# Kernel optimization log

Measured on AMD Instinct MI355X. Metric: run time of the kernel, lower is better.

The kernel has to match this reference:

```python
import jax, jax.numpy as jnp
import numpy as np

B, S = 2, 1024
V, D, H, L, F, M = 50257, 768, 12, 6, 3072, 1024
DK = D // H
EPS = 1e-5


def _layer_norm(x, g, b):
    mu = jnp.mean(x, axis=-1, keepdims=True)
    var = jnp.mean(jnp.square(x - mu), axis=-1, keepdims=True)
    return (x - mu) * jax.lax.rsqrt(var + EPS) * g + b


def setup_inputs() -> dict:
    key = jax.random.key(0)
    ks = jax.random.split(key, 20)
    std = 0.02
    inp = {
        'input_ids': jax.random.randint(ks[0], (B, S), 0, V),
        'tok_emb': jax.random.normal(ks[1], (V, D), jnp.float32) * std,
        'pos_emb': jax.random.normal(ks[2], (M, D), jnp.float32) * std,
        # per-layer stacked params; linear weights stored as [in, out] (y = x @ W)
        'wq': jax.random.normal(ks[3], (L, D, D), jnp.float32) * std,
        'wk': jax.random.normal(ks[4], (L, D, D), jnp.float32) * std,
        'wv': jax.random.normal(ks[5], (L, D, D), jnp.float32) * std,
        'wo': jax.random.normal(ks[6], (L, D, D), jnp.float32) * std,
        'bo': jnp.zeros((L, D), jnp.float32),
        'fc_w': jax.random.normal(ks[7], (L, D, F), jnp.float32) * std,
        'fc_b': jnp.zeros((L, F), jnp.float32),
        'proj_w': jax.random.normal(ks[8], (L, F, D), jnp.float32) * std,
        'proj_b': jnp.zeros((L, D), jnp.float32),
        'ln1_g': jnp.ones((L, D), jnp.float32),
        'ln1_b': jnp.zeros((L, D), jnp.float32),
        'ln2_g': jnp.ones((L, D), jnp.float32),
        'ln2_b': jnp.zeros((L, D), jnp.float32),
        'lnf_g': jnp.ones((D,), jnp.float32),
        'lnf_b': jnp.zeros((D,), jnp.float32),
        'out_w': jax.random.normal(ks[9], (D, V), jnp.float32) * std,
    }
    return inp


def reference(input_ids, tok_emb, pos_emb, wq, wk, wv, wo, bo, fc_w, fc_b,
              proj_w, proj_b, ln1_g, ln1_b, ln2_g, ln2_b, lnf_g, lnf_b, out_w):
    b, s = input_ids.shape
    x = tok_emb[input_ids] + pos_emb[jnp.arange(s)][None, :, :]  # [B,S,D]
    causal = jnp.tril(jnp.ones((s, s), bool))  # [S,S]
    scale = 1.0 / np.sqrt(DK)
    for l in range(L):
        xn = _layer_norm(x, ln1_g[l], ln1_b[l])
        q = (xn @ wq[l]).reshape(b, s, H, DK).transpose(0, 2, 1, 3)
        k = (xn @ wk[l]).reshape(b, s, H, DK).transpose(0, 2, 1, 3)
        v = (xn @ wv[l]).reshape(b, s, H, DK).transpose(0, 2, 1, 3)
        scores = jnp.einsum('bhqd,bhkd->bhqk', q, k) * scale
        scores = jnp.where(causal[None, None], scores, -1e9)
        attn = jax.nn.softmax(scores, axis=-1)
        ctx = jnp.einsum('bhqk,bhkd->bhqd', attn, v)
        ctx = ctx.transpose(0, 2, 1, 3).reshape(b, s, D)
        x = x + ctx @ wo[l] + bo[l]
        xn = _layer_norm(x, ln2_g[l], ln2_b[l])
        h = jax.nn.gelu(xn @ fc_w[l] + fc_b[l], approximate=False)
        x = x + h @ proj_w[l] + proj_b[l]
    x = _layer_norm(x, lnf_g, lnf_b)
    logits = x @ out_w  # [B,S,V]
    return logits
```

## Files before the change

### kernel.cpp

```cpp
#include <hip/hip_runtime.h>
#include <hip/hip_bf16.h>
#include <math.h>

#define BB 2
#define SS 1024
#define DD 768
#define HH 12
#define LL 6
#define FF 3072
#define VV 50257
#define DKK 64
#define NROWS (BB * SS)
#define QKVN (3 * DD)
#define QBLK 64
#define KVBLK 64
#define VPAD 50432

#define OFF_QKV 0
#define OFF_WO  1769472
#define OFF_FC  2359296
#define OFF_PROJ 4718592
#define PL      7077888

typedef __attribute__((ext_vector_type(8))) short short8v;
typedef __attribute__((ext_vector_type(4))) float f32x4;
typedef __attribute__((ext_vector_type(4))) int int4v;

__device__ __forceinline__ float gelu_f(float x) {
    return 0.5f * x * (1.0f + erff(x * 0.70710678118654752440f));
}

__device__ __forceinline__ void gload16(const void* g, void* l) {
    __builtin_amdgcn_global_load_lds(
        (const __attribute__((address_space(1))) void*)g,
        (__attribute__((address_space(3))) void*)l, 16, 0, 0);
}
__device__ __forceinline__ unsigned lds_off(const void* p) {
    return (unsigned)(size_t)(const __attribute__((address_space(3))) char*)p;
}
__device__ __forceinline__ short8v ds_read128(unsigned addr) {
    short8v r;
    asm volatile("ds_read_b128 %0, %1" : "=v"(r) : "v"(addr));
    return r;
}

__global__ __launch_bounds__(256) void embed_kernel(
    const int* __restrict__ ids, const float* __restrict__ tok,
    const float* __restrict__ pos, float* __restrict__ x) {
    int row = blockIdx.x;
    int s = row & (SS - 1);
    int id = ids[row];
    const float* t = tok + (size_t)id * DD;
    const float* p = pos + (size_t)s * DD;
    float* xr = x + (size_t)row * DD;
    for (int i = threadIdx.x; i < DD; i += 256)
        xr[i] = t[i] + p[i];
}

__global__ __launch_bounds__(256) void ln_kernel(
    const float* __restrict__ x, const float* __restrict__ g,
    const float* __restrict__ b, float* __restrict__ out) {
    int row = blockIdx.x;
    int tid = threadIdx.x;
    const float* xr = x + (size_t)row * DD;
    float v0 = xr[tid], v1 = xr[tid + 256], v2 = xr[tid + 512];
    __shared__ float red[256];
    red[tid] = v0 + v1 + v2;
    __syncthreads();
    for (int s2 = 128; s2 > 0; s2 >>= 1) {
        if (tid < s2) red[tid] += red[tid + s2];
        __syncthreads();
    }
    float mu = red[0] * (1.0f / DD);
    __syncthreads();
    float d0 = v0 - mu, d1 = v1 - mu, d2 = v2 - mu;
    red[tid] = d0 * d0 + d1 * d1 + d2 * d2;
    __syncthreads();
    for (int s2 = 128; s2 > 0; s2 >>= 1) {
        if (tid < s2) red[tid] += red[tid + s2];
        __syncthreads();
    }
    float r = rsqrtf(red[0] * (1.0f / DD) + 1e-5f);
    float* o = out + (size_t)row * DD;
    o[tid]       = d0 * r * g[tid]       + b[tid];
    o[tid + 256] = d1 * r * g[tid + 256] + b[tid + 256];
    o[tid + 512] = d2 * r * g[tid + 512] + b[tid + 512];
}

__global__ __launch_bounds__(256) void ln_bf16_kernel(
    const float* __restrict__ x, const float* __restrict__ g,
    const float* __restrict__ b, __hip_bfloat16* __restrict__ out) {
    int row = blockIdx.x;
    int tid = threadIdx.x;
    const float* xr = x + (size_t)row * DD;
    float v0 = xr[tid], v1 = xr[tid + 256], v2 = xr[tid + 512];
    __shared__ float red[256];
    red[tid] = v0 + v1 + v2;
    __syncthreads();
    for (int s2 = 128; s2 > 0; s2 >>= 1) {
        if (tid < s2) red[tid] += red[tid + s2];
        __syncthreads();
    }
    float mu = red[0] * (1.0f / DD);
    __syncthreads();
    float d0 = v0 - mu, d1 = v1 - mu, d2 = v2 - mu;
    red[tid] = d0 * d0 + d1 * d1 + d2 * d2;
    __syncthreads();
    for (int s2 = 128; s2 > 0; s2 >>= 1) {
        if (tid < s2) red[tid] += red[tid + s2];
        __syncthreads();
    }
    float r = rsqrtf(red[0] * (1.0f / DD) + 1e-5f);
    __hip_bfloat16* o = out + (size_t)row * DD;
    o[tid]       = __float2bfloat16(d0 * r * g[tid]       + b[tid]);
    o[tid + 256] = __float2bfloat16(d1 * r * g[tid + 256] + b[tid + 256]);
    o[tid + 512] = __float2bfloat16(d2 * r * g[tid + 512] + b[tid + 512]);
}

__global__ __launch_bounds__(256) void transpose_cvt_kernel(
    const float* __restrict__ W, __hip_bfloat16* __restrict__ Wt, int K, int N) {
    __shared__ float t[32][33];
    int bn = blockIdx.x * 32, bk = blockIdx.y * 32;
    int tx = threadIdx.x & 31, ty = threadIdx.x >> 5;
    for (int r = ty; r < 32; r += 8)
        t[r][tx] = (bn + tx < N) ? W[(size_t)(bk + r) * N + bn + tx] : 0.0f;
    __syncthreads();
    for (int r = ty; r < 32; r += 8) {
        int n = bn + r;
        if (n < N) Wt[(size_t)n * K + bk + tx] = __float2bfloat16(t[tx][r]);
    }
}

__global__ __launch_bounds__(256) void transpose_all_kernel(
    const float* __restrict__ wq, const float* __restrict__ wk,
    const float* __restrict__ wv, const float* __restrict__ wo,
    const float* __restrict__ fc_w, const float* __restrict__ proj_w,
    const float* __restrict__ out_w, __hip_bfloat16* __restrict__ Wt_all) {
    int bid = blockIdx.x;
    const float* W;
    __hip_bfloat16* Wt;
    int K, N, tn, tk;
    if (bid < 6 * 6912) {
        int l = bid / 6912, r = bid % 6912;
        __hip_bfloat16* base = Wt_all + (size_t)l * PL;
        if (r < 1728) {
            int which = r / 576, idx = r % 576;
            W = (which == 0 ? wq : (which == 1 ? wk : wv)) + (size_t)l * DD * DD;
            Wt = base + (size_t)which * DD * DD;
            K = DD; N = DD; tn = idx % 24; tk = idx / 24;
        } else if (r < 2304) {
            int idx = r - 1728;
            W = wo + (size_t)l * DD * DD;
            Wt = base + OFF_WO;
            K = DD; N = DD; tn = idx % 24; tk = idx / 24;
        } else if (r < 4608) {
            int idx = r - 2304;
            W = fc_w + (size_t)l * DD * FF;
            Wt = base + OFF_FC;
            K = DD; N = FF; tn = idx % 96; tk = idx / 96;
        } else {
            int idx = r - 4608;
            W = proj_w + (size_t)l * FF * DD;
            Wt = base + OFF_PROJ;
            K = FF; N = DD; tn = idx % 24; tk = idx / 24;
        }
    } else {
        int idx = bid - 6 * 6912;
        W = out_w;
        Wt = Wt_all + (size_t)6 * PL;
        K = DD; N = VV; tn = idx % 1571; tk = idx / 1571;
    }
    __shared__ float t[32][33];
    int bn = tn * 32, bk = tk * 32;
    int tx = threadIdx.x & 31, ty = threadIdx.x >> 5;
    for (int r = ty; r < 32; r += 8)
        t[r][tx] = (bn + tx < N) ? W[(size_t)(bk + r) * N + bn + tx] : 0.0f;
    __syncthreads();
    for (int r = ty; r < 32; r += 8) {
        int n = bn + r;
        if (n < N) Wt[(size_t)n * K + bk + tx] = __float2bfloat16(t[tx][r]);
    }
}

#define LDSOFF(row, ks) (((row) * 64) + ((((ks) ^ (((row) >> 1) & 3))) << 4))
#define SWZ128(row, byteoff) \
    ((row) * 128 + (((((byteoff) >> 4) ^ ((row) & 7)) & 7) << 4) + ((byteoff) & 15))

__device__ __forceinline__ void tile_remap(int mtiles, int BM, int BN, int& bm, int& bn) {
    const int nblk = gridDim.x;
    int hw = blockIdx.x, j = hw;
    if ((nblk & 7) == 0) j = (hw & 7) * (nblk >> 3) + (hw >> 3);
    bm = (j % mtiles) * BM;
    bn = (j / mtiles) * BN;
}

__global__ __launch_bounds__(512) void gemm256_kernel(
    const __hip_bfloat16* __restrict__ A, const __hip_bfloat16* __restrict__ Wt,
    const float* __restrict__ bias, float* __restrict__ Cf,
    __hip_bfloat16* __restrict__ Cb, int M, int N, int K, int do_gelu, int mtiles) {
    __shared__ __align__(16) char lds[131072];
    const int tid = threadIdx.x;
    const int lane = tid & 63;
    const int w = tid >> 6;
    const int wr = w >> 2, wc = w & 3;
    const int r16 = lane & 15, kg = lane >> 4;
    int bm, bn;
    tile_remap(mtiles, 256, 256, bm, bn);

    auto STAGE = [&](int T) {
        char* lb = lds + (T & 3) * 32768;
        int k0 = T * 32;
#pragma unroll
        for (int u = 0; u < 2; ++u) {
            int cb = w * 128 + u * 64;
            int c = cb + lane;
            int row = c >> 2;
            int sc = ((c & 3) ^ ((row >> 1) & 3)) * 8;
            gload16(A + (size_t)(bm + row) * K + k0 + sc, lb + cb * 16);
            gload16(Wt + (size_t)(bn + row) * K + k0 + sc, lb + 16384 + cb * 16);
        }
    };

    f32x4 acc[8][4];
    const f32x4 zf = {0.0f, 0.0f, 0.0f, 0.0f};
#pragma unroll
    for (int i = 0; i < 8; ++i)
#pragma unroll
        for (int j = 0; j < 4; ++j) acc[i][j] = zf;

    unsigned aoff[8], boff[4];
#pragma unroll
    for (int i = 0; i < 8; ++i) aoff[i] = LDSOFF(wr * 128 + i * 16 + r16, kg);
#pragma unroll
    for (int j = 0; j < 4; ++j) boff[j] = 16384 + LDSOFF(wc * 64 + j * 16 + r16, kg);
    const unsigned lbase = lds_off(lds);

    STAGE(0); STAGE(1); STAGE(2);
    const int NT = K >> 5;
    for (int t = 0; t < NT; ++t) {
        if (t < NT - 2)       asm volatile("s_waitcnt vmcnt(8)" ::: "memory");
        else if (t == NT - 2) asm volatile("s_waitcnt vmcnt(4)" ::: "memory");
        else                  asm volatile("s_waitcnt vmcnt(0)" ::: "memory");
        __builtin_amdgcn_s_barrier();
        __builtin_amdgcn_sched_barrier(0);
        if (t + 3 < NT) STAGE(t + 3);
        unsigned ab = lbase + (unsigned)(t & 3) * 32768u;
        short8v bf[4], af[8];
#pragma unroll
        for (int j = 0; j < 4; ++j) bf[j] = ds_read128(ab + boff[j]);
#pragma unroll
        for (int i = 0; i < 8; ++i) af[i] = ds_read128(ab + aoff[i]);
#pragma unroll
        for (int i = 0; i < 8; ++i) {
            asm volatile("s_waitcnt lgkmcnt(%0)" :: "i"(7 - i) : "memory");
            __builtin_amdgcn_sched_barrier(0);
#pragma unroll
            for (int j = 0; j < 4; ++j)
                acc[i][j] = __builtin_amdgcn_mfma_f32_16x16x32_bf16(
                    af[i], bf[j], acc[i][j], 0, 0, 0);
        }
    }

    const int rg = lane >> 4;
#pragma unroll
    for (int i = 0; i < 8; ++i)
#pragma unroll
        for (int j = 0; j < 4; ++j) {
            int col = bn + wc * 64 + j * 16 + r16;
            if (col < N) {
#pragma unroll
                for (int r = 0; r < 4; ++r) {
                    int row = bm + wr * 128 + i * 16 + rg * 4 + r;
                    float v = acc[i][j][r];
                    if (bias) v += bias[col];
                    if (do_gelu) v = gelu_f(v);
                    if (Cf) Cf[(size_t)row * N + col] = v;
                    else Cb[(size_t)row * N + col] = __float2bfloat16(v);
                }
            }
        }
}

template<int BM, int BN>
__global__ __launch_bounds__(256) void gemm_mfma_kernel(
    const __hip_bfloat16* __restrict__ A, const __hip_bfloat16* __restrict__ Wt,
    const float* __restrict__ bias, const float* __restrict__ residual,
    float* __restrict__ Cf, __hip_bfloat16* __restrict__ Cb,
    int M, int N, int K, int do_gelu, int mtiles) {
    constexpr int BK = 32;
    constexpr int UA = (BM * 4) / 256;
    constexpr int UB = (BN * 4) / 256;
    constexpr int FM = BM / 32;
    constexpr int FN = BN / 32;
    __shared__ __align__(16) char As[BM * 64];
    __shared__ __align__(16) char Bs[BN * 64];

    const int tid = threadIdx.x;
    const int lane = tid & 63;
    const int wid = tid >> 6;
    int bm, bn;
    tile_remap(mtiles, BM, BN, bm, bn);
    const int r16 = lane & 15;
    const int kg = lane >> 4;
    const int wm = (wid >> 1) * (FM * 16);
    const int wn = (wid & 1) * (FN * 16);

    f32x4 acc[FM][FN];
    const f32x4 zf = {0.0f, 0.0f, 0.0f, 0.0f};
#pragma unroll
    for (int i = 0; i < FM; ++i)
#pragma unroll
        for (int j = 0; j < FN; ++j) acc[i][j] = zf;

    int4v areg[UA], breg[UB];
    const int4v zi = {0, 0, 0, 0};

#pragma unroll
    for (int u = 0; u < UA; ++u) {
        int c = tid + u * 256, row = c >> 2, sl = c & 3;
        areg[u] = *(const int4v*)(A + (size_t)(bm + row) * K + sl * 8);
    }
#pragma unroll
    for (int u = 0; u < UB; ++u) {
        int c = tid + u * 256, row = c >> 2, sl = c & 3;
        int4v bv = zi;
        if (bn + row < N) bv = *(const int4v*)(Wt + (size_t)(bn + row) * K + sl * 8);
        breg[u] = bv;
    }

    for (int k0 = 0; k0 < K; k0 += BK) {
        __syncthreads();
#pragma unroll
        for (int u = 0; u < UA; ++u) {
            int c = tid + u * 256, row = c >> 2, sl = c & 3;
            *(int4v*)(As + LDSOFF(row, sl)) = areg[u];
        }
#pragma unroll
        for (int u = 0; u < UB; ++u) {
            int c = tid + u * 256, row = c >> 2, sl = c & 3;
            *(int4v*)(Bs + LDSOFF(row, sl)) = breg[u];
        }
        __syncthreads();
        int kn = k0 + BK;
        if (kn < K) {
#pragma unroll
            for (int u = 0; u < UA; ++u) {
                int c = tid + u * 256, row = c >> 2, sl = c & 3;
                areg[u] = *(const int4v*)(A + (size_t)(bm + row) * K + kn + sl * 8);
            }
#pragma unroll
            for (int u = 0; u < UB; ++u) {
                int c = tid + u * 256, row = c >> 2, sl = c & 3;
                int4v bv = zi;
                if (bn + row < N) bv = *(const int4v*)(Wt + (size_t)(bn + row) * K + kn + sl * 8);
                breg[u] = bv;
            }
        }
        short8v af[FM], bfr[FN];
#pragma unroll
        for (int i = 0; i < FM; ++i) {
            int row = wm + i * 16 + r16;
            af[i] = *(const short8v*)(As + LDSOFF(row, kg));
        }
#pragma unroll
        for (int j = 0; j < FN; ++j) {
            int row = wn + j * 16 + r16;
            bfr[j] = *(const short8v*)(Bs + LDSOFF(row, kg));
        }
#pragma unroll
        for (int i = 0; i < FM; ++i)
#pragma unroll
            for (int j = 0; j < FN; ++j)
                acc[i][j] = __builtin_amdgcn_mfma_f32_16x16x32_bf16(
                    af[i], bfr[j], acc[i][j], 0, 0, 0);
    }

    const int rg = lane >> 4;
#pragma unroll
    for (int i = 0; i < FM; ++i) {
#pragma unroll
        for (int j = 0; j < FN; ++j) {
            int col = bn + wn + j * 16 + r16;
            if (col < N) {
#pragma unroll
                for (int r = 0; r < 4; ++r) {
                    int row = bm + wm + i * 16 + rg * 4 + r;
                    float v = acc[i][j][r];
                    if (bias) v += bias[col];
                    if (do_gelu) v = gelu_f(v);
                    size_t o = (size_t)row * N + col;
                    if (residual) v += residual[o];
                    if (Cf) Cf[o] = v;
                    else Cb[o] = __float2bfloat16(v);
                }
            }
        }
    }
}

__global__ __launch_bounds__(256) void qkv_gemm_kernel(
    const __hip_bfloat16* __restrict__ A, const __hip_bfloat16* __restrict__ Wt,
    __hip_bfloat16* __restrict__ qh, __hip_bfloat16* __restrict__ kh,
    __hip_bfloat16* __restrict__ vt) {
    constexpr int BM = 128, BN = 128, BK = 32;
    constexpr int K = DD;
    constexpr int FM = 4, FN = 4;
    __shared__ __align__(16) char As[BM * 64];
    __shared__ __align__(16) char Bs[BN * 64];

    const int tid = threadIdx.x;
    const int lane = tid & 63;
    const int wid = tid >> 6;
    int bm, bn;
    tile_remap(16, BM, BN, bm, bn);
    const int r16 = lane & 15;
    const int kg = lane >> 4;
    const int wm = (wid >> 1) * 64;
    const int wn = (wid & 1) * 64;

    f32x4 acc[FM][FN];
    const f32x4 zf = {0.0f, 0.0f, 0.0f, 0.0f};
#pragma unroll
    for (int i = 0; i < FM; ++i)
#pragma unroll
        for (int j = 0; j < FN; ++j) acc[i][j] = zf;

    int4v areg[2], breg[2];
#pragma unroll
    for (int u = 0; u < 2; ++u) {
        int c = tid + u * 256, row = c >> 2, sl = c & 3;
        areg[u] = *(const int4v*)(A + (size_t)(bm + row) * K + sl * 8);
        breg[u] = *(const int4v*)(Wt + (size_t)(bn + row) * K + sl * 8);
    }

    for (int k0 = 0; k0 < K; k0 += BK) {
        __syncthreads();
#pragma unroll
        for (int u = 0; u < 2; ++u) {
            int c = tid + u * 256, row = c >> 2, sl = c & 3;
            *(int4v*)(As + LDSOFF(row, sl)) = areg[u];
            *(int4v*)(Bs + LDSOFF(row, sl)) = breg[u];
        }
        __syncthreads();
        int kn = k0 + BK;
        if (kn < K) {
#pragma unroll
            for (int u = 0; u < 2; ++u) {
                int c = tid + u * 256, row = c >> 2, sl = c & 3;
                areg[u] = *(const int4v*)(A + (size_t)(bm + row) * K + kn + sl * 8);
                breg[u] = *(const int4v*)(Wt + (size_t)(bn + row) * K + kn + sl * 8);
            }
        }
        short8v af[FM], bfr[FN];
#pragma unroll
        for (int i = 0; i < FM; ++i)
            af[i] = *(const short8v*)(As + LDSOFF(wm + i * 16 + r16, kg));
#pragma unroll
        for (int j = 0; j < FN; ++j)
            bfr[j] = *(const short8v*)(Bs + LDSOFF(wn + j * 16 + r16, kg));
#pragma unroll
        for (int i = 0; i < FM; ++i)
#pragma unroll
            for (int j = 0; j < FN; ++j)
                acc[i][j] = __builtin_amdgcn_mfma_f32_16x16x32_bf16(
                    af[i], bfr[j], acc[i][j], 0, 0, 0);
    }

#pragma unroll
    for (int i = 0; i < FM; ++i) {
#pragma unroll
        for (int j = 0; j < FN; ++j) {
            int col = bn + wn + j * 16 + r16;
#pragma unroll
            for (int r = 0; r < 4; ++r) {
                int row = bm + wm + i * 16 + kg * 4 + r;
                int b = row >> 10, s = row & (SS - 1);
                float v = acc[i][j][r];
                if (col < DD) {
                    int h = col >> 6, d = col & 63;
                    qh[((size_t)(b * HH + h) * SS + s) * DKK + d] =
                        __float2bfloat16(v * 0.125f);
                } else if (col < 2 * DD) {
                    int c = col - DD, h = c >> 6, d = c & 63;
                    kh[((size_t)(b * HH + h) * SS + s) * DKK + d] = __float2bfloat16(v);
                } else {
                    int c = col - 2 * DD, h = c >> 6, d = c & 63;
                    vt[((size_t)(b * HH + h) * DKK + d) * SS + s] = __float2bfloat16(v);
                }
            }
        }
    }
}

__global__ __launch_bounds__(256) void flash_attn_kernel(
    const __hip_bfloat16* __restrict__ qh, const __hip_bfloat16* __restrict__ kh,
    const __hip_bfloat16* __restrict__ vt, __hip_bfloat16* __restrict__ ctx) {
    __shared__ __align__(16) char Ks[KVBLK * 128];
    __shared__ __align__(16) char Vs[DKK * 128];
    __shared__ __align__(16) char Ps[4][16 * 128];

    const int bh = blockIdx.x;
    const int qt = (gridDim.y - 1) - blockIdx.y;
    const int q0 = qt * QBLK;
    const int b = bh / HH;
    const int h = bh - b * HH;
    const int tid = threadIdx.x;
    const int lane = tid & 63;
    const int w = tid >> 6;
    const int r16 = lane & 15;
    const int kg = lane >> 4;
    char* Pw = Ps[w];

    const size_t qbase = ((size_t)bh * SS + q0 + w * 16 + r16) * DKK;
    short8v qf0 = *(const short8v*)(qh + qbase + kg * 8);
    short8v qf1 = *(const short8v*)(qh + qbase + 32 + kg * 8);

    f32x4 acc_o[4];
    const f32x4 zf = {0.0f, 0.0f, 0.0f, 0.0f};
    float m[4], l[4];
#pragma unroll
    for (int j = 0; j < 4; ++j) acc_o[j] = zf;
#pragma unroll
    for (int r = 0; r < 4; ++r) { m[r] = -1e30f; l[r] = 0.0f; }

    const int nt = qt + 1;
    for (int t = 0; t < nt; ++t) {
        __syncthreads();
        {
            const __hip_bfloat16* kp = kh + ((size_t)bh * SS + t * KVBLK) * DKK;
            const __hip_bfloat16* vp = vt + (size_t)bh * DKK * SS + t * KVBLK;
#pragma unroll
            for (int u = 0; u < 2; ++u) {
                int c = tid + u * 256;
                int row = c >> 3, slot = c & 7;
                *(int4v*)(Ks + SWZ128(row, slot * 16)) =
                    *(const int4v*)(kp + (size_t)row * DKK + slot * 8);
                *(int4v*)(Vs + SWZ128(row, slot * 16)) =
                    *(const int4v*)(vp + (size_t)row * SS + slot * 8);
            }
        }
        __syncthreads();

        f32x4 s[4];
#pragma unroll
        for (int j = 0; j < 4; ++j) s[j] = zf;
#pragma unroll
        for (int j = 0; j < 4; ++j) {
            short8v k0f = *(const short8v*)(Ks + SWZ128(j * 16 + r16, kg * 16));
            short8v k1f = *(const short8v*)(Ks + SWZ128(j * 16 + r16, 64 + kg * 16));
            s[j] = __builtin_amdgcn_mfma_f32_16x16x32_bf16(qf0, k0f, s[j], 0, 0, 0);
            s[j] = __builtin_amdgcn_mfma_f32_16x16x32_bf16(qf1, k1f, s[j], 0, 0, 0);
        }

        if (t == qt) {
#pragma unroll
            for (int j = 0; j < 4; ++j)
#pragma unroll
                for (int r = 0; r < 4; ++r)
                    if (j * 16 + r16 > w * 16 + kg * 4 + r) s[j][r] = -1e30f;
        }

        float alpha[4], rsum[4];
#pragma unroll
        for (int r = 0; r < 4; ++r) {
            float v = fmaxf(fmaxf(s[0][r], s[1][r]), fmaxf(s[2][r], s[3][r]));
#pragma unroll
            for (int d2 = 1; d2 < 16; d2 <<= 1)
                v = fmaxf(v, __shfl_xor(v, d2));
            float mnew = fmaxf(m[r], v);
            alpha[r] = __expf(m[r] - mnew);
            m[r] = mnew;
            rsum[r] = 0.0f;
        }
#pragma unroll
        for (int j = 0; j < 4; ++j)
#pragma unroll
            for (int r = 0; r < 4; ++r) {
                float p = __expf(s[j][r] - m[r]);
                rsum[r] += p;
                *(__hip_bfloat16*)(Pw + SWZ128(kg * 4 + r, (j * 16 + r16) * 2)) =
                    __float2bfloat16(p);
            }
#pragma unroll
        for (int r = 0; r < 4; ++r) {
#pragma unroll
            for (int d2 = 1; d2 < 16; d2 <<= 1)
                rsum[r] += __shfl_xor(rsum[r], d2);
            l[r] = l[r] * alpha[r] + rsum[r];
        }
#pragma unroll
        for (int j = 0; j < 4; ++j)
#pragma unroll
            for (int r = 0; r < 4; ++r) acc_o[j][r] *= alpha[r];

        short8v pa0 = *(const short8v*)(Pw + SWZ128(r16, kg * 16));
        short8v pa1 = *(const short8v*)(Pw + SWZ128(r16, 64 + kg * 16));
#pragma unroll
        for (int j = 0; j < 4; ++j) {
            short8v v0f = *(const short8v*)(Vs + SWZ128(j * 16 + r16, kg * 16));
            short8v v1f = *(const short8v*)(Vs + SWZ128(j * 16 + r16, 64 + kg * 16));
            acc_o[j] = __builtin_amdgcn_mfma_f32_16x16x32_bf16(pa0, v0f, acc_o[j], 0, 0, 0);
            acc_o[j] = __builtin_amdgcn_mfma_f32_16x16x32_bf16(pa1, v1f, acc_o[j], 0, 0, 0);
        }
    }

#pragma unroll
    for (int r = 0; r < 4; ++r) {
        float inv = 1.0f / l[r];
        int row = q0 + w * 16 + kg * 4 + r;
        __hip_bfloat16* cp = ctx + ((size_t)(b * SS) + row) * DD + h * DKK;
#pragma unroll
        for (int j = 0; j < 4; ++j)
            cp[j * 16 + r16] = __float2bfloat16(acc_o[j][r] * inv);
    }
}

__global__ __launch_bounds__(256) void gemm_kernel(
    const float* __restrict__ A, const float* __restrict__ W,
    const float* __restrict__ bias, const float* __restrict__ residual,
    float* __restrict__ C, int M, int N, int K, int do_gelu) {
    __shared__ float As[16][64];
    __shared__ float Ws[16][68];
    int tid = threadIdx.x;
    int bn = blockIdx.x * 64, bm = blockIdx.y * 64;
    int tx = tid & 15, ty = tid >> 4;
    int ar = tid >> 2, ak = (tid & 3) << 2;
    int wr = tid >> 4, wc = (tid & 15) << 2;
    bool n_vec = ((N & 3) == 0);
    float acc[4][4] = {};
    for (int k0 = 0; k0 < K; k0 += 16) {
        float4 av = *(const float4*)&A[(size_t)(bm + ar) * K + (k0 + ak)];
        As[ak + 0][ar] = av.x; As[ak + 1][ar] = av.y;
        As[ak + 2][ar] = av.z; As[ak + 3][ar] = av.w;
        int gn = bn + wc;
        const float* wp = &W[(size_t)(k0 + wr) * N + gn];
        float w0, w1, w2, w3;
        if (n_vec && gn + 3 < N) {
            float4 wv4 = *(const float4*)wp;
            w0 = wv4.x; w1 = wv4.y; w2 = wv4.z; w3 = wv4.w;
        } else {
            w0 = (gn + 0 < N) ? wp[0] : 0.0f;
            w1 = (gn + 1 < N) ? wp[1] : 0.0f;
            w2 = (gn + 2 < N) ? wp[2] : 0.0f;
            w3 = (gn + 3 < N) ? wp[3] : 0.0f;
        }
        Ws[wr][wc + 0] = w0; Ws[wr][wc + 1] = w1;
        Ws[wr][wc + 2] = w2; Ws[wr][wc + 3] = w3;
        __syncthreads();
#pragma unroll
        for (int kk = 0; kk < 16; ++kk) {
            float a[4], w[4];
#pragma unroll
            for (int i = 0; i < 4; ++i) a[i] = As[kk][ty * 4 + i];
#pragma unroll
            for (int j = 0; j < 4; ++j) w[j] = Ws[kk][tx * 4 + j];
#pragma unroll
            for (int i = 0; i < 4; ++i)
#pragma unroll
                for (int j = 0; j < 4; ++j)
                    acc[i][j] = fmaf(a[i], w[j], acc[i][j]);
        }
        __syncthreads();
    }
#pragma unroll
    for (int i = 0; i < 4; ++i) {
        int row = bm + ty * 4 + i;
#pragma unroll
        for (int j = 0; j < 4; ++j) {
            int col = bn + tx * 4 + j;
            if (col < N) {
                float val = acc[i][j];
                if (bias) val += bias[col];
                if (do_gelu) val = gelu_f(val);
                if (residual) val += residual[(size_t)row * N + col];
                C[(size_t)row * N + col] = val;
            }
        }
    }
}

__global__ __launch_bounds__(256) void attn_kernel(
    const float* __restrict__ q, const float* __restrict__ k,
    const float* __restrict__ v, float* __restrict__ ctx) {
    int bid = blockIdx.x;
    int qi = bid & (SS - 1);
    int bh = bid >> 10;
    int h = bh % HH;
    int b = bh / HH;
    int tid = threadIdx.x;
    __shared__ float qs[DKK];
    __shared__ float p[SS];
    __shared__ float red[256];
    __shared__ float ctx_red[4][DKK];
    const float* qrow = q + ((size_t)(b * SS + qi)) * DD + h * DKK;
    if (tid < DKK) qs[tid] = qrow[tid];
    __syncthreads();
    int nk = qi + 1;
    const float scale = 0.125f;
    for (int ki = tid; ki < nk; ki += 256) {
        const float* krow = k + ((size_t)(b * SS + ki)) * DD + h * DKK;
        float dot = 0.0f;
#pragma unroll
        for (int d = 0; d < DKK; d += 4) {
            float4 kv = *(const float4*)&krow[d];
            dot += qs[d] * kv.x + qs[d + 1] * kv.y + qs[d + 2] * kv.z + qs[d + 3] * kv.w;
        }
        p[ki] = dot * scale;
    }
    __syncthreads();
    float lmax = -1e30f;
    for (int ki = tid; ki < nk; ki += 256) lmax = fmaxf(lmax, p[ki]);
    red[tid] = lmax;
    __syncthreads();
    for (int s2 = 128; s2 > 0; s2 >>= 1) {
        if (tid < s2) red[tid] = fmaxf(red[tid], red[tid + s2]);
        __syncthreads();
    }
    float mm = red[0];
    __syncthreads();
    float lsum = 0.0f;
    for (int ki = tid; ki < nk; ki += 256) {
        float e = __expf(p[ki] - mm);
        p[ki] = e;
        lsum += e;
    }
    red[tid] = lsum;
    __syncthreads();
    for (int s2 = 128; s2 > 0; s2 >>= 1) {
        if (tid < s2) red[tid] += red[tid + s2];
        __syncthreads();
    }
    float inv = 1.0f / red[0];
    int d = tid & 63;
    int chunk = tid >> 6;
    float accd = 0.0f;
    for (int ki = chunk; ki < nk; ki += 4)
        accd += p[ki] * v[((size_t)(b * SS + ki)) * DD + h * DKK + d];
    ctx_red[chunk][d] = accd;
    __syncthreads();
    if (tid < DKK) {
        float sum = (ctx_red[0][tid] + ctx_red[1][tid]) + (ctx_red[2][tid] + ctx_red[3][tid]);
        ctx[((size_t)(b * SS + qi)) * DD + h * DKK + tid] = sum * inv;
    }
}

extern "C" void kernel_launch(void* const* d_in, const int* in_sizes, int n_in,
                              void* d_out, int out_size, void* d_ws, size_t ws_size,
                              hipStream_t stream) {
    const int*   ids    = (const int*)  d_in[0];
    const float* tok    = (const float*)d_in[1];
    const float* pos    = (const float*)d_in[2];
    const float* wq     = (const float*)d_in[3];
    const float* wk     = (const float*)d_in[4];
    const float* wv     = (const float*)d_in[5];
    const float* wo     = (const float*)d_in[6];
    const float* bo     = (const float*)d_in[7];
    const float* fc_w   = (const float*)d_in[8];
    const float* fc_b   = (const float*)d_in[9];
    const float* proj_w = (const float*)d_in[10];
    const float* proj_b = (const float*)d_in[11];
    const float* ln1_g  = (const float*)d_in[12];
    const float* ln1_b  = (const float*)d_in[13];
    const float* ln2_g  = (const float*)d_in[14];
    const float* ln2_b  = (const float*)d_in[15];
    const float* lnf_g  = (const float*)d_in[16];
    const float* lnf_b  = (const float*)d_in[17];
    const float* out_w  = (const float*)d_in[18];
    float* out = (float*)d_out;

    dim3 blk(256);

    const size_t SZ_X    = (size_t)NROWS * DD * 4;
    const size_t SZ_XN   = (size_t)NROWS * DD * 2;
    const size_t SZ_HD   = (size_t)BB * HH * SS * DKK * 2;
    const size_t SZ_CTX  = (size_t)NROWS * DD * 2;
    const size_t SZ_H    = (size_t)NROWS * FF * 2;
    const size_t SZ_WT1  = (size_t)VPAD * DD * 2;
    const size_t SZ_WTA  = ((size_t)6 * PL + (size_t)VPAD * DD) * 2;
    const size_t ACT     = SZ_X + SZ_XN + 3 * SZ_HD + SZ_CTX + SZ_H;
    const size_t NEED_MID = ACT + SZ_WT1;
    const size_t NEED_BIG = ACT + SZ_WTA;

    if (ws_size >= NEED_MID) {
        const bool big = (ws_size >= NEED_BIG);
        char* p = (char*)d_ws;
        float*          x    = (float*)p;          p += SZ_X;
        __hip_bfloat16* xn   = (__hip_bfloat16*)p; p += SZ_XN;
        __hip_bfloat16* qhb  = (__hip_bfloat16*)p; p += SZ_HD;
        __hip_bfloat16* khb  = (__hip_bfloat16*)p; p += SZ_HD;
        __hip_bfloat16* vtb  = (__hip_bfloat16*)p; p += SZ_HD;
        __hip_bfloat16* ctx  = (__hip_bfloat16*)p; p += SZ_CTX;
        __hip_bfloat16* hbuf = (__hip_bfloat16*)p; p += SZ_H;
        __hip_bfloat16* Wt   = (__hip_bfloat16*)p;

        dim3 tD(DD / 32, DD / 32);
        dim3 tF(FF / 32, DD / 32);
        dim3 tP(DD / 32, FF / 32);
        dim3 tV((VV + 31) / 32, DD / 32);

        const int nQKV = (QKVN / 128) * (NROWS / 128);
        const int nWO  = (DD / 64) * (NROWS / 64);
        const int nFC  = (FF / 128) * (NROWS / 128);
        const int nV   = (VPAD / 256) * (NROWS / 256);
        dim3 gA(BB * HH, SS / QBLK);

        if (big)
            transpose_all_kernel<<<6 * 6912 + 37704, blk, 0, stream>>>(
                wq, wk, wv, wo, fc_w, proj_w, out_w, Wt);

        embed_kernel<<<NROWS, blk, 0, stream>>>(ids, tok, pos, x);

        for (int l = 0; l < LL; ++l) {
            __hip_bfloat16* qkvWt = big ? Wt + (size_t)l * PL : Wt;
            __hip_bfloat16* woWt  = big ? Wt + (size_t)l * PL + OFF_WO : Wt;
            __hip_bfloat16* fcWt  = big ? Wt + (size_t)l * PL + OFF_FC : Wt;
            __hip_bfloat16* pjWt  = big ? Wt + (size_t)l * PL + OFF_PROJ : Wt;

            ln_bf16_kernel<<<NROWS, blk, 0, stream>>>(x, ln1_g + l * DD, ln1_b + l * DD, xn);
            if (!big) {
                transpose_cvt_kernel<<<tD, blk, 0, stream>>>(wq + (size_t)l * DD * DD, qkvWt, DD, DD);
                transpose_cvt_kernel<<<tD, blk, 0, stream>>>(wk + (size_t)l * DD * DD, qkvWt + (size_t)DD * DD, DD, DD);
                transpose_cvt_kernel<<<tD, blk, 0, stream>>>(wv + (size_t)l * DD * DD, qkvWt + (size_t)2 * DD * DD, DD, DD);
            }
            qkv_gemm_kernel<<<nQKV, blk, 0, stream>>>(xn, qkvWt, qhb, khb, vtb);
            flash_attn_kernel<<<gA, blk, 0, stream>>>(qhb, khb, vtb, ctx);
            if (!big)
                transpose_cvt_kernel<<<tD, blk, 0, stream>>>(wo + (size_t)l * DD * DD, woWt, DD, DD);
            gemm_mfma_kernel<64, 64><<<nWO, blk, 0, stream>>>(
                ctx, woWt, bo + l * DD, x, x, nullptr, NROWS, DD, DD, 0, NROWS / 64);
            ln_bf16_kernel<<<NROWS, blk, 0, stream>>>(x, ln2_g + l * DD, ln2_b + l * DD, xn);
            if (!big)
                transpose_cvt_kernel<<<tF, blk, 0, stream>>>(fc_w + (size_t)l * DD * FF, fcWt, DD, FF);
            gemm_mfma_kernel<128, 128><<<nFC, blk, 0, stream>>>(
                xn, fcWt, fc_b + l * FF, nullptr, nullptr, hbuf, NROWS, FF, DD, 1, NROWS / 128);
            if (!big)
                transpose_cvt_kernel<<<tP, blk, 0, stream>>>(proj_w + (size_t)l * FF * DD, pjWt, FF, DD);
            gemm_mfma_kernel<64, 64><<<nWO, blk, 0, stream>>>(
                hbuf, pjWt, proj_b + l * DD, x, x, nullptr, NROWS, DD, FF, 0, NROWS / 64);
        }

        __hip_bfloat16* outWt = big ? Wt + (size_t)6 * PL : Wt;
        ln_bf16_kernel<<<NROWS, blk, 0, stream>>>(x, lnf_g, lnf_b, xn);
        if (!big)
            transpose_cvt_kernel<<<tV, blk, 0, stream>>>(out_w, outWt, DD, VV);
        gemm256_kernel<<<nV, 512, 0, stream>>>(
            xn, outWt, nullptr, out, nullptr, NROWS, VV, DD, 0, NROWS / 256);
        return;
    }

    const size_t XSZ = (size_t)NROWS * DD;
    float* ws = (float*)d_ws;
    float* x  = ws;
    float* xn = x  + XSZ;
    float* qb = xn + XSZ;
    float* kb = qb + XSZ;
    float* vb = kb + XSZ;
    float* cb = vb + XSZ;
    float* hb = cb + XSZ;

    dim3 gD((DD + 63) / 64, NROWS / 64);
    dim3 gF((FF + 63) / 64, NROWS / 64);
    dim3 gV2((VV + 63) / 64, NROWS / 64);

    embed_kernel<<<NROWS, blk, 0, stream>>>(ids, tok, pos, x);
    for (int l = 0; l < LL; ++l) {
        const float* wq_l = wq + (size_t)l * DD * DD;
        const float* wk_l = wk + (size_t)l * DD * DD;
        const float* wv_l = wv + (size_t)l * DD * DD;
        const float* wo_l = wo + (size_t)l * DD * DD;
        const float* fc_w_l = fc_w + (size_t)l * DD * FF;
        const float* pj_w_l = proj_w + (size_t)l * FF * DD;
        ln_kernel<<<NROWS, blk, 0, stream>>>(x, ln1_g + l * DD, ln1_b + l * DD, xn);
        gemm_kernel<<<gD, blk, 0, stream>>>(xn, wq_l, nullptr, nullptr, qb, NROWS, DD, DD, 0);
        gemm_kernel<<<gD, blk, 0, stream>>>(xn, wk_l, nullptr, nullptr, kb, NROWS, DD, DD, 0);
        gemm_kernel<<<gD, blk, 0, stream>>>(xn, wv_l, nullptr, nullptr, vb, NROWS, DD, DD, 0);
        attn_kernel<<<BB * HH * SS, blk, 0, stream>>>(qb, kb, vb, cb);
        gemm_kernel<<<gD, blk, 0, stream>>>(cb, wo_l, bo + l * DD, x, x, NROWS, DD, DD, 0);
        ln_kernel<<<NROWS, blk, 0, stream>>>(x, ln2_g + l * DD, ln2_b + l * DD, xn);
        gemm_kernel<<<gF, blk, 0, stream>>>(xn, fc_w_l, fc_b + l * FF, nullptr, hb, NROWS, FF, DD, 1);
        gemm_kernel<<<gD, blk, 0, stream>>>(hb, pj_w_l, proj_b + l * DD, x, x, NROWS, DD, FF, 0);
    }
    ln_kernel<<<NROWS, blk, 0, stream>>>(x, lnf_g, lnf_b, xn);
    gemm_kernel<<<gV2, blk, 0, stream>>>(xn, out_w, nullptr, nullptr, out, NROWS, VV, DD, 0);
}
```

Baseline: 1.532 ms.

## Load flash-attention K/V fragments directly from global; batch GEMM LDS reads before MFMAs

The flash attention kernel stops staging K and V tiles through shared memory. Each wave now reads its MFMA operand fragments straight from global memory, which removes the two block barriers per KV tile. The cost is that each of the four waves re-fetches the same K/V data, which relies on the cache, and the loads are exposed with no prefetch. Separately, the bf16 GEMM main loop issues all LDS fragment reads and waits for them all once, instead of waiting incrementally per A fragment, which reduces overlap of LDS latency with MFMA work.

Result: slower. 1.728 ms (+12.8%).

```diff
diff --git a/kernel.cpp b/kernel.cpp
--- a/kernel.cpp
+++ b/kernel.cpp
@@ -245,20 +245,19 @@
         __builtin_amdgcn_sched_barrier(0);
         if (t + 3 < NT) STAGE(t + 3);
         unsigned ab = lbase + (unsigned)(t & 3) * 32768u;
-        short8v bf[4], af[8];
+        short8v af[8], bf[4];
+#pragma unroll
+        for (int i = 0; i < 8; ++i) af[i] = ds_read128(ab + aoff[i]);
 #pragma unroll
         for (int j = 0; j < 4; ++j) bf[j] = ds_read128(ab + boff[j]);
-#pragma unroll
-        for (int i = 0; i < 8; ++i) af[i] = ds_read128(ab + aoff[i]);
-#pragma unroll
-        for (int i = 0; i < 8; ++i) {
-            asm volatile("s_waitcnt lgkmcnt(%0)" :: "i"(7 - i) : "memory");
-            __builtin_amdgcn_sched_barrier(0);
+        asm volatile("s_waitcnt lgkmcnt(0)" ::: "memory");
+        __builtin_amdgcn_sched_barrier(0);
+#pragma unroll
+        for (int i = 0; i < 8; ++i)
 #pragma unroll
             for (int j = 0; j < 4; ++j)
                 acc[i][j] = __builtin_amdgcn_mfma_f32_16x16x32_bf16(
                     af[i], bf[j], acc[i][j], 0, 0, 0);
-        }
     }
 
     const int rg = lane >> 4;
@@ -495,8 +494,6 @@
 __global__ __launch_bounds__(256) void flash_attn_kernel(
     const __hip_bfloat16* __restrict__ qh, const __hip_bfloat16* __restrict__ kh,
     const __hip_bfloat16* __restrict__ vt, __hip_bfloat16* __restrict__ ctx) {
-    __shared__ __align__(16) char Ks[KVBLK * 128];
-    __shared__ __align__(16) char Vs[DKK * 128];
     __shared__ __align__(16) char Ps[4][16 * 128];
 
     const int bh = blockIdx.x;
@@ -515,6 +512,9 @@
     short8v qf0 = *(const short8v*)(qh + qbase + kg * 8);
     short8v qf1 = *(const short8v*)(qh + qbase + 32 + kg * 8);
 
+    const __hip_bfloat16* kbase = kh + (size_t)bh * SS * DKK;
+    const __hip_bfloat16* vbase = vt + (size_t)bh * DKK * SS;
+
     f32x4 acc_o[4];
     const f32x4 zf = {0.0f, 0.0f, 0.0f, 0.0f};
     float m[4], l[4];
@@ -525,29 +525,14 @@
 
     const int nt = qt + 1;
     for (int t = 0; t < nt; ++t) {
-        __syncthreads();
-        {
-            const __hip_bfloat16* kp = kh + ((size_t)bh * SS + t * KVBLK) * DKK;
-            const __hip_bfloat16* vp = vt + (size_t)bh * DKK * SS + t * KVBLK;
-#pragma unroll
-            for (int u = 0; u < 2; ++u) {
-                int c = tid + u * 256;
-                int row = c >> 3, slot = c & 7;
-                *(int4v*)(Ks + SWZ128(row, slot * 16)) =
-                    *(const int4v*)(kp + (size_t)row * DKK + slot * 8);
-                *(int4v*)(Vs + SWZ128(row, slot * 16)) =
-                    *(const int4v*)(vp + (size_t)row * SS + slot * 8);
-            }
-        }
-        __syncthreads();
-
         f32x4 s[4];
 #pragma unroll
         for (int j = 0; j < 4; ++j) s[j] = zf;
 #pragma unroll
         for (int j = 0; j < 4; ++j) {
-            short8v k0f = *(const short8v*)(Ks + SWZ128(j * 16 + r16, kg * 16));
-            short8v k1f = *(const short8v*)(Ks + SWZ128(j * 16 + r16, 64 + kg * 16));
+            const __hip_bfloat16* kp = kbase + (size_t)(t * KVBLK + j * 16 + r16) * DKK;
+            short8v k0f = *(const short8v*)(kp + kg * 8);
+            short8v k1f = *(const short8v*)(kp + 32 + kg * 8);
             s[j] = __builtin_amdgcn_mfma_f32_16x16x32_bf16(qf0, k0f, s[j], 0, 0, 0);
             s[j] = __builtin_amdgcn_mfma_f32_16x16x32_bf16(qf1, k1f, s[j], 0, 0, 0);
         }
@@ -597,8 +582,9 @@
         short8v pa1 = *(const short8v*)(Pw + SWZ128(r16, 64 + kg * 16));
 #pragma unroll
         for (int j = 0; j < 4; ++j) {
-            short8v v0f = *(const short8v*)(Vs + SWZ128(j * 16 + r16, kg * 16));
-            short8v v1f = *(const short8v*)(Vs + SWZ128(j * 16 + r16, 64 + kg * 16));
+            const __hip_bfloat16* vp = vbase + (size_t)(j * 16 + r16) * SS + t * KVBLK;
+            short8v v0f = *(const short8v*)(vp + kg * 8);
+            short8v v1f = *(const short8v*)(vp + 32 + kg * 8);
             acc_o[j] = __builtin_amdgcn_mfma_f32_16x16x32_bf16(pa0, v0f, acc_o[j], 0, 0, 0);
             acc_o[j] = __builtin_amdgcn_mfma_f32_16x16x32_bf16(pa1, v1f, acc_o[j], 0, 0, 0);
         }
```

## Port QKV and FC GEMMs to 4-stage direct-to-LDS pipelined 128x128 kernel

Applied to the files above, without the earlier changes.

Adds a 128x128 GEMM that stages tiles with async global-to-LDS loads in a four-deep ring buffer with swizzled columns. It is used for the FC GEMM, and the QKV projection is rewritten the same way. The previous register-staged double-sync loop is removed. The 256 kernel's inner loop also changes: it now waits for all LDS reads before issuing MFMAs instead of waiting per fragment row. The cost is 64KB of LDS per block, which may reduce occupancy.

New measurement: 1.486 ms. 1.03x faster.

```diff
diff --git a/kernel.cpp b/kernel.cpp
--- a/kernel.cpp
+++ b/kernel.cpp
@@ -245,20 +245,19 @@
         __builtin_amdgcn_sched_barrier(0);
         if (t + 3 < NT) STAGE(t + 3);
         unsigned ab = lbase + (unsigned)(t & 3) * 32768u;
-        short8v bf[4], af[8];
+        short8v af[8], bf[4];
+#pragma unroll
+        for (int i = 0; i < 8; ++i) af[i] = ds_read128(ab + aoff[i]);
 #pragma unroll
         for (int j = 0; j < 4; ++j) bf[j] = ds_read128(ab + boff[j]);
-#pragma unroll
-        for (int i = 0; i < 8; ++i) af[i] = ds_read128(ab + aoff[i]);
-#pragma unroll
-        for (int i = 0; i < 8; ++i) {
-            asm volatile("s_waitcnt lgkmcnt(%0)" :: "i"(7 - i) : "memory");
-            __builtin_amdgcn_sched_barrier(0);
+        asm volatile("s_waitcnt lgkmcnt(0)" ::: "memory");
+        __builtin_amdgcn_sched_barrier(0);
+#pragma unroll
+        for (int i = 0; i < 8; ++i)
 #pragma unroll
             for (int j = 0; j < 4; ++j)
                 acc[i][j] = __builtin_amdgcn_mfma_f32_16x16x32_bf16(
                     af[i], bf[j], acc[i][j], 0, 0, 0);
-        }
     }
 
     const int rg = lane >> 4;
@@ -279,6 +278,183 @@
                 }
             }
         }
+}
+
+__global__ __launch_bounds__(256) void gemm128_kernel(
+    const __hip_bfloat16* __restrict__ A, const __hip_bfloat16* __restrict__ Wt,
+    const float* __restrict__ bias, float* __restrict__ Cf,
+    __hip_bfloat16* __restrict__ Cb, int M, int N, int K, int do_gelu, int mtiles) {
+    __shared__ __align__(16) char lds[65536];
+    const int tid = threadIdx.x;
+    const int lane = tid & 63;
+    const int w = tid >> 6;
+    const int wr = w >> 1, wc = w & 1;
+    const int r16 = lane & 15, kg = lane >> 4;
+    int bm, bn;
+    tile_remap(mtiles, 128, 128, bm, bn);
+
+    auto STAGE = [&](int T) {
+        char* lb = lds + (T & 3) * 16384;
+        int k0 = T * 32;
+#pragma unroll
+        for (int u = 0; u < 2; ++u) {
+            int cb = w * 128 + u * 64;
+            int c = cb + lane;
+            int row = c >> 2;
+            int sc = ((c & 3) ^ ((row >> 1) & 3)) * 8;
+            gload16(A + (size_t)(bm + row) * K + k0 + sc, lb + cb * 16);
+            gload16(Wt + (size_t)(bn + row) * K + k0 + sc, lb + 8192 + cb * 16);
+        }
+    };
+
+    f32x4 acc[4][4];
+    const f32x4 zf = {0.0f, 0.0f, 0.0f, 0.0f};
+#pragma unroll
+    for (int i = 0; i < 4; ++i)
+#pragma unroll
+        for (int j = 0; j < 4; ++j) acc[i][j] = zf;
+
+    unsigned aoff[4], boff[4];
+#pragma unroll
+    for (int i = 0; i < 4; ++i) aoff[i] = LDSOFF(wr * 64 + i * 16 + r16, kg);
+#pragma unroll
+    for (int j = 0; j < 4; ++j) boff[j] = 8192 + LDSOFF(wc * 64 + j * 16 + r16, kg);
+    const unsigned lbase = lds_off(lds);
+
+    STAGE(0); STAGE(1); STAGE(2);
+    const int NT = K >> 5;
+    for (int t = 0; t < NT; ++t) {
+        if (t < NT - 2)       asm volatile("s_waitcnt vmcnt(8)" ::: "memory");
+        else if (t == NT - 2) asm volatile("s_waitcnt vmcnt(4)" ::: "memory");
+        else                  asm volatile("s_waitcnt vmcnt(0)" ::: "memory");
+        __builtin_amdgcn_s_barrier();
+        __builtin_amdgcn_sched_barrier(0);
+        if (t + 3 < NT) STAGE(t + 3);
+        unsigned ab = lbase + (unsigned)(t & 3) * 16384u;
+        short8v af[4], bf[4];
+#pragma unroll
+        for (int i = 0; i < 4; ++i) af[i] = ds_read128(ab + aoff[i]);
+#pragma unroll
+        for (int j = 0; j < 4; ++j) bf[j] = ds_read128(ab + boff[j]);
+        asm volatile("s_waitcnt lgkmcnt(0)" ::: "memory");
+        __builtin_amdgcn_sched_barrier(0);
+#pragma unroll
+        for (int i = 0; i < 4; ++i)
+#pragma unroll
+            for (int j = 0; j < 4; ++j)
+                acc[i][j] = __builtin_amdgcn_mfma_f32_16x16x32_bf16(
+                    af[i], bf[j], acc[i][j], 0, 0, 0);
+    }
+
+    const int rg = lane >> 4;
+#pragma unroll
+    for (int i = 0; i < 4; ++i)
+#pragma unroll
+        for (int j = 0; j < 4; ++j) {
+            int col = bn + wc * 64 + j * 16 + r16;
+#pragma unroll
+            for (int r = 0; r < 4; ++r) {
+                int row = bm + wr * 64 + i * 16 + rg * 4 + r;
+                float v = acc[i][j][r];
+                if (bias) v += bias[col];
+                if (do_gelu) v = gelu_f(v);
+                if (Cf) Cf[(size_t)row * N + col] = v;
+                else Cb[(size_t)row * N + col] = __float2bfloat16(v);
+            }
+        }
+}
+
+__global__ __launch_bounds__(256) void qkv_gemm_kernel(
+    const __hip_bfloat16* __restrict__ A, const __hip_bfloat16* __restrict__ Wt,
+    __hip_bfloat16* __restrict__ qh, __hip_bfloat16* __restrict__ kh,
+    __hip_bfloat16* __restrict__ vt) {
+    constexpr int K = DD;
+    __shared__ __align__(16) char lds[65536];
+    const int tid = threadIdx.x;
+    const int lane = tid & 63;
+    const int w = tid >> 6;
+    const int wr = w >> 1, wc = w & 1;
+    const int r16 = lane & 15, kg = lane >> 4;
+    int bm, bn;
+    tile_remap(16, 128, 128, bm, bn);
+
+    auto STAGE = [&](int T) {
+        char* lb = lds + (T & 3) * 16384;
+        int k0 = T * 32;
+#pragma unroll
+        for (int u = 0; u < 2; ++u) {
+            int cb = w * 128 + u * 64;
+            int c = cb + lane;
+            int row = c >> 2;
+            int sc = ((c & 3) ^ ((row >> 1) & 3)) * 8;
+            gload16(A + (size_t)(bm + row) * K + k0 + sc, lb + cb * 16);
+            gload16(Wt + (size_t)(bn + row) * K + k0 + sc, lb + 8192 + cb * 16);
+        }
+    };
+
+    f32x4 acc[4][4];
+    const f32x4 zf = {0.0f, 0.0f, 0.0f, 0.0f};
+#pragma unroll
+    for (int i = 0; i < 4; ++i)
+#pragma unroll
+        for (int j = 0; j < 4; ++j) acc[i][j] = zf;
+
+    unsigned aoff[4], boff[4];
+#pragma unroll
+    for (int i = 0; i < 4; ++i) aoff[i] = LDSOFF(wr * 64 + i * 16 + r16, kg);
+#pragma unroll
+    for (int j = 0; j < 4; ++j) boff[j] = 8192 + LDSOFF(wc * 64 + j * 16 + r16, kg);
+    const unsigned lbase = lds_off(lds);
+
+    STAGE(0); STAGE(1); STAGE(2);
+    const int NT = K >> 5;
+    for (int t = 0; t < NT; ++t) {
+        if (t < NT - 2)       asm volatile("s_waitcnt vmcnt(8)" ::: "memory");
+        else if (t == NT - 2) asm volatile("s_waitcnt vmcnt(4)" ::: "memory");
+        else                  asm volatile("s_waitcnt vmcnt(0)" ::: "memory");
+        __builtin_amdgcn_s_barrier();
+        __builtin_amdgcn_sched_barrier(0);
+        if (t + 3 < NT) STAGE(t + 3);
+        unsigned ab = lbase + (unsigned)(t & 3) * 16384u;
+        short8v af[4], bf[4];
+#pragma unroll
+        for (int i = 0; i < 4; ++i) af[i] = ds_read128(ab + aoff[i]);
+#pragma unroll
+        for (int j = 0; j < 4; ++j) bf[j] = ds_read128(ab + boff[j]);
+        asm volatile("s_waitcnt lgkmcnt(0)" ::: "memory");
+        __builtin_amdgcn_sched_barrier(0);
+#pragma unroll
+        for (int i = 0; i < 4; ++i)
+#pragma unroll
+            for (int j = 0; j < 4; ++j)
+                acc[i][j] = __builtin_amdgcn_mfma_f32_16x16x32_bf16(
+                    af[i], bf[j], acc[i][j], 0, 0, 0);
+    }
+
+#pragma unroll
+    for (int i = 0; i < 4; ++i) {
+#pragma unroll
+        for (int j = 0; j < 4; ++j) {
+            int col = bn + wc * 64 + j * 16 + r16;
+#pragma unroll
+            for (int r = 0; r < 4; ++r) {
+                int row = bm + wr * 64 + i * 16 + kg * 4 + r;
+                int b = row >> 10, s = row & (SS - 1);
+                float v = acc[i][j][r];
+                if (col < DD) {
+                    int h = col >> 6, d = col & 63;
+                    qh[((size_t)(b * HH + h) * SS + s) * DKK + d] =
+                        __float2bfloat16(v * 0.125f);
+                } else if (col < 2 * DD) {
+                    int c = col - DD, h = c >> 6, d = c & 63;
+                    kh[((size_t)(b * HH + h) * SS + s) * DKK + d] = __float2bfloat16(v);
+                } else {
+                    int c = col - 2 * DD, h = c >> 6, d = c & 63;
+                    vt[((size_t)(b * HH + h) * DKK + d) * SS + s] = __float2bfloat16(v);
+                }
+            }
+        }
+    }
 }
 
 template<int BM, int BN>
@@ -392,100 +568,6 @@
                     if (residual) v += residual[o];
                     if (Cf) Cf[o] = v;
                     else Cb[o] = __float2bfloat16(v);
-                }
-            }
-        }
-    }
-}
-
-__global__ __launch_bounds__(256) void qkv_gemm_kernel(
-    const __hip_bfloat16* __restrict__ A, const __hip_bfloat16* __restrict__ Wt,
-    __hip_bfloat16* __restrict__ qh, __hip_bfloat16* __restrict__ kh,
-    __hip_bfloat16* __restrict__ vt) {
-    constexpr int BM = 128, BN = 128, BK = 32;
-    constexpr int K = DD;
-    constexpr int FM = 4, FN = 4;
-    __shared__ __align__(16) char As[BM * 64];
-    __shared__ __align__(16) char Bs[BN * 64];
-
-    const int tid = threadIdx.x;
-    const int lane = tid & 63;
-    const int wid = tid >> 6;
-    int bm, bn;
-    tile_remap(16, BM, BN, bm, bn);
-    const int r16 = lane & 15;
-    const int kg = lane >> 4;
-    const int wm = (wid >> 1) * 64;
-    const int wn = (wid & 1) * 64;
-
-    f32x4 acc[FM][FN];
-    const f32x4 zf = {0.0f, 0.0f, 0.0f, 0.0f};
-#pragma unroll
-    for (int i = 0; i < FM; ++i)
-#pragma unroll
-        for (int j = 0; j < FN; ++j) acc[i][j] = zf;
-
-    int4v areg[2], breg[2];
-#pragma unroll
-    for (int u = 0; u < 2; ++u) {
-        int c = tid + u * 256, row = c >> 2, sl = c & 3;
-        areg[u] = *(const int4v*)(A + (size_t)(bm + row) * K + sl * 8);
-        breg[u] = *(const int4v*)(Wt + (size_t)(bn + row) * K + sl * 8);
-    }
-
-    for (int k0 = 0; k0 < K; k0 += BK) {
-        __syncthreads();
-#pragma unroll
-        for (int u = 0; u < 2; ++u) {
-            int c = tid + u * 256, row = c >> 2, sl = c & 3;
-            *(int4v*)(As + LDSOFF(row, sl)) = areg[u];
-            *(int4v*)(Bs + LDSOFF(row, sl)) = breg[u];
-        }
-        __syncthreads();
-        int kn = k0 + BK;
-        if (kn < K) {
-#pragma unroll
-            for (int u = 0; u < 2; ++u) {
-                int c = tid + u * 256, row = c >> 2, sl = c & 3;
-                areg[u] = *(const int4v*)(A + (size_t)(bm + row) * K + kn + sl * 8);
-                breg[u] = *(const int4v*)(Wt + (size_t)(bn + row) * K + kn + sl * 8);
-            }
-        }
-        short8v af[FM], bfr[FN];
-#pragma unroll
-        for (int i = 0; i < FM; ++i)
-            af[i] = *(const short8v*)(As + LDSOFF(wm + i * 16 + r16, kg));
-#pragma unroll
-        for (int j = 0; j < FN; ++j)
-            bfr[j] = *(const short8v*)(Bs + LDSOFF(wn + j * 16 + r16, kg));
-#pragma unroll
-        for (int i = 0; i < FM; ++i)
-#pragma unroll
-            for (int j = 0; j < FN; ++j)
-                acc[i][j] = __builtin_amdgcn_mfma_f32_16x16x32_bf16(
-                    af[i], bfr[j], acc[i][j], 0, 0, 0);
-    }
-
-#pragma unroll
-    for (int i = 0; i < FM; ++i) {
-#pragma unroll
-        for (int j = 0; j < FN; ++j) {
-            int col = bn + wn + j * 16 + r16;
-#pragma unroll
-            for (int r = 0; r < 4; ++r) {
-                int row = bm + wm + i * 16 + kg * 4 + r;
-                int b = row >> 10, s = row & (SS - 1);
-                float v = acc[i][j][r];
-                if (col < DD) {
-                    int h = col >> 6, d = col & 63;
-                    qh[((size_t)(b * HH + h) * SS + s) * DKK + d] =
-                        __float2bfloat16(v * 0.125f);
-                } else if (col < 2 * DD) {
-                    int c = col - DD, h = c >> 6, d = c & 63;
-                    kh[((size_t)(b * HH + h) * SS + s) * DKK + d] = __float2bfloat16(v);
-                } else {
-                    int c = col - 2 * DD, h = c >> 6, d = c & 63;
-                    vt[((size_t)(b * HH + h) * DKK + d) * SS + s] = __float2bfloat16(v);
                 }
             }
         }
@@ -831,8 +913,8 @@
             ln_bf16_kernel<<<NROWS, blk, 0, stream>>>(x, ln2_g + l * DD, ln2_b + l * DD, xn);
             if (!big)
                 transpose_cvt_kernel<<<tF, blk, 0, stream>>>(fc_w + (size_t)l * DD * FF, fcWt, DD, FF);
-            gemm_mfma_kernel<128, 128><<<nFC, blk, 0, stream>>>(
-                xn, fcWt, fc_b + l * FF, nullptr, nullptr, hbuf, NROWS, FF, DD, 1, NROWS / 128);
+            gemm128_kernel<<<nFC, blk, 0, stream>>>(
+                xn, fcWt, fc_b + l * FF, nullptr, hbuf, NROWS, FF, DD, 1, NROWS / 128);
             if (!big)
                 transpose_cvt_kernel<<<tP, blk, 0, stream>>>(proj_w + (size_t)l * FF * DD, pjWt, FF, DD);
             gemm_mfma_kernel<64, 64><<<nWO, blk, 0, stream>>>(
```
